# Kernel optimization log

Measured on AMD Instinct MI355X. Metric: run time of the kernel, lower is better.

The kernel has to match this reference:

```python
import jax, jax.numpy as jnp
import numpy as np

NV = 20000; NC = 20000; E = 500000
IN_SHAPE = 2; PE_DIM = 8; HID = 64; NL = 3
EPS = 1e-7  # GENConv message eps


def _lin(x, w, b):
    return x @ w + b


def _encode(x, pe, ew, eb, pw1, pb1, pw2, pb2):
    # relu(cat([Linear(x), 0.5*(pe_mlp(pe)+pe_mlp(-pe))], dim=1))
    def pe_mlp(p):
        return _lin(jax.nn.relu(_lin(p, pw1, pb1)), pw2, pb2)
    h = jnp.concatenate([_lin(x, ew, eb), 0.5 * (pe_mlp(pe) + pe_mlp(-pe))], axis=1)
    return jax.nn.relu(h)


def _genconv(x_src, x_dst, src, dst, ewt, lew, leb, w1, b1, w2, b2, n_dst):
    # GENConv(aggr='softmax', t=1, norm=None, msg_norm=False, edge_dim=1)
    msg = jax.nn.relu(x_src[src] + _lin(ewt, lew, leb)) + EPS  # [E, HID]
    m = jax.ops.segment_max(msg, dst, num_segments=n_dst)      # stable segment softmax
    ex = jnp.exp(msg - m[dst])
    s = jax.ops.segment_sum(ex, dst, num_segments=n_dst)
    agg = jax.ops.segment_sum(ex / (s[dst] + 1e-16) * msg, dst, num_segments=n_dst)
    out = agg + x_dst
    return _lin(jax.nn.relu(_lin(out, w1, b1)), w2, b2)  # MLP [hid -> 2hid -> hid]


def setup_inputs() -> dict:
    key = jax.random.key(0)
    ks = iter(jax.random.split(key, 64))
    d = {}
    d['x_vals'] = jax.random.normal(next(ks), (NV, IN_SHAPE), jnp.float32)
    d['x_cons'] = jax.random.normal(next(ks), (NC, IN_SHAPE), jnp.float32)
    d['pe_vals'] = jax.random.normal(next(ks), (NV, PE_DIM), jnp.float32)
    d['pe_cons'] = jax.random.normal(next(ks), (NC, PE_DIM), jnp.float32)
    d['edge_index_v2c'] = jnp.stack([
        jax.random.randint(next(ks), (E,), 0, NV),
        jax.random.randint(next(ks), (E,), 0, NC)])
    d['edge_index_c2v'] = jnp.stack([
        jax.random.randint(next(ks), (E,), 0, NC),
        jax.random.randint(next(ks), (E,), 0, NV)])
    d['edge_weight_v2c'] = jax.random.normal(next(ks), (E, 1), jnp.float32)
    d['edge_weight_c2v'] = jax.random.normal(next(ks), (E, 1), jnp.float32)
    def p(shape):
        return jax.random.normal(next(ks), shape, jnp.float32) * 0.05
    for k_ in ['vals', 'cons']:
        d[f'enc_{k_}_w'] = p((IN_SHAPE, HID // 2)); d[f'enc_{k_}_b'] = p((HID // 2,))
        d[f'pe_{k_}_w1'] = p((PE_DIM, HID)); d[f'pe_{k_}_b1'] = p((HID,))
        d[f'pe_{k_}_w2'] = p((HID, HID // 2)); d[f'pe_{k_}_b2'] = p((HID // 2,))
    for c in ['v2c', 'c2v']:
        d[f'{c}_edge_w'] = p((NL, 1, HID)); d[f'{c}_edge_b'] = p((NL, HID))
        d[f'{c}_w1'] = p((NL, HID, 2 * HID)); d[f'{c}_b1'] = p((NL, 2 * HID))
        d[f'{c}_w2'] = p((NL, 2 * HID, HID)); d[f'{c}_b2'] = p((NL, HID))
    for k_ in ['vals', 'cons']:
        d[f'pred_{k_}_w1'] = p((HID, HID)); d[f'pred_{k_}_b1'] = p((HID,))
        d[f'pred_{k_}_w2'] = p((HID, 1)); d[f'pred_{k_}_b2'] = p((1,))
    return d


def reference(x_vals, x_cons, pe_vals, pe_cons, edge_index_v2c, edge_index_c2v,
              edge_weight_v2c, edge_weight_c2v,
              enc_vals_w, enc_vals_b, pe_vals_w1, pe_vals_b1, pe_vals_w2, pe_vals_b2,
              enc_cons_w, enc_cons_b, pe_cons_w1, pe_cons_b1, pe_cons_w2, pe_cons_b2,
              v2c_edge_w, v2c_edge_b, v2c_w1, v2c_b1, v2c_w2, v2c_b2,
              c2v_edge_w, c2v_edge_b, c2v_w1, c2v_b1, c2v_w2, c2v_b2,
              pred_vals_w1, pred_vals_b1, pred_vals_w2, pred_vals_b2,
              pred_cons_w1, pred_cons_b1, pred_cons_w2, pred_cons_b2):
    vals = _encode(x_vals, pe_vals, enc_vals_w, enc_vals_b,
                   pe_vals_w1, pe_vals_b1, pe_vals_w2, pe_vals_b2)
    cons = _encode(x_cons, pe_cons, enc_cons_w, enc_cons_b,
                   pe_cons_w1, pe_cons_b1, pe_cons_w2, pe_cons_b2)
    hv, hc = [], []
    for i in range(NL):
        cons = _genconv(vals, cons, edge_index_v2c[0], edge_index_v2c[1],
                        edge_weight_v2c, v2c_edge_w[i], v2c_edge_b[i],
                        v2c_w1[i], v2c_b1[i], v2c_w2[i], v2c_b2[i], NC)
        vals = _genconv(cons, vals, edge_index_c2v[0], edge_index_c2v[1],
                        edge_weight_c2v, c2v_edge_w[i], c2v_edge_b[i],
                        c2v_w1[i], c2v_b1[i], c2v_w2[i], c2v_b2[i], NV)
        hc.append(cons); hv.append(vals)
    V = jnp.stack(hv)  # [NL, NV, HID]
    C = jnp.stack(hc)  # [NL, NC, HID]
    pv = _lin(jax.nn.relu(_lin(V, pred_vals_w1, pred_vals_b1)), pred_vals_w2, pred_vals_b2)
    pc = _lin(jax.nn.relu(_lin(C, pred_cons_w1, pred_cons_b1)), pred_cons_w2, pred_cons_b2)
    return pv[..., 0].T, pc[..., 0].T  # [NV, NL], [NC, NL]
```

## Files before the change

kernel.cpp:

```cpp
#include <hip/hip_runtime.h>

#define NVN 20000
#define NCN 20000
#define NE  500000
#define HID 64
#define NLAYER 3
#define TN 40
#define BSH 8
#define NB 79
#define P1E 2048

__device__ __forceinline__ float relu_(float x) { return fmaxf(x, 0.0f); }

__global__ __launch_bounds__(256) void binhist_kernel(
    const int* __restrict__ dstA, const int* __restrict__ dstB,
    int* __restrict__ binszA, int* __restrict__ binszB)
{
    __shared__ int cA[NB], cB[NB];
    int t = threadIdx.x;
    int e0 = blockIdx.x * P1E;
    if (t < NB) { cA[t] = 0; cB[t] = 0; }
    __syncthreads();
    for (int i = t; i < P1E; i += 256) {
        int e = e0 + i;
        if (e < NE) {
            atomicAdd(&cA[dstA[e] >> BSH], 1);
            atomicAdd(&cB[dstB[e] >> BSH], 1);
        }
    }
    __syncthreads();
    if (t < NB) {
        if (cA[t] > 0) atomicAdd(&binszA[t], cA[t]);
        if (cB[t] > 0) atomicAdd(&binszB[t], cB[t]);
    }
}

__global__ __launch_bounds__(256) void binscan_kernel(
    const int* __restrict__ binszA, int* __restrict__ binbaseA, int* __restrict__ bincurA,
    const int* __restrict__ binszB, int* __restrict__ binbaseB, int* __restrict__ bincurB)
{
    const int* binsz = blockIdx.x ? binszB : binszA;
    int* binbase     = blockIdx.x ? binbaseB : binbaseA;
    int* bincur      = blockIdx.x ? bincurB : bincurA;
    __shared__ int p[256];
    int t = threadIdx.x;
    p[t] = (t < NB) ? binsz[t] : 0;
    __syncthreads();
    for (int off = 1; off < 256; off <<= 1) {
        int v = (t >= off) ? p[t - off] : 0;
        __syncthreads();
        p[t] += v;
        __syncthreads();
    }
    if (t < NB) { int b = (t == 0) ? 0 : p[t - 1]; binbase[t] = b; bincur[t] = b; }
    if (t == NB) binbase[NB] = p[NB - 1];
}

__global__ __launch_bounds__(256) void scatter_p1_kernel(
    const int* __restrict__ eiA, const float* __restrict__ ewA,
    int* __restrict__ bincurA, int2* __restrict__ stageA,
    const int* __restrict__ eiB, const float* __restrict__ ewB,
    int* __restrict__ bincurB, int2* __restrict__ stageB)
{
    __shared__ int rnk[P1E];
    __shared__ int cnt[NB], base_[NB];
    int t = threadIdx.x;
    int e0 = blockIdx.x * P1E;

    for (int g = 0; g < 2; ++g) {
        const int* ei   = g ? eiB : eiA;
        const float* ew = g ? ewB : ewA;
        int* bincur     = g ? bincurB : bincurA;
        int2* stage     = g ? stageB : stageA;

        if (t < NB) cnt[t] = 0;
        __syncthreads();
        for (int i = t; i < P1E; i += 256) {
            int e = e0 + i;
            if (e < NE) {
                int d = ei[NE + e];
                rnk[i] = atomicAdd(&cnt[d >> BSH], 1);
            }
        }
        __syncthreads();
        if (t < NB && cnt[t] > 0) base_[t] = atomicAdd(&bincur[t], cnt[t]);
        __syncthreads();
        for (int i = t; i < P1E; i += 256) {
            int e = e0 + i;
            if (e < NE) {
                int s = ei[e], d = ei[NE + e];
                float w = ew[e];
                stage[base_[d >> BSH] + rnk[i]] =
                    make_int2((int)((unsigned)s | ((unsigned)d << 16)), __float_as_int(w));
            }
        }
        __syncthreads();
    }
}

__global__ __launch_bounds__(1024) void scatter_p2_kernel(
    const int* __restrict__ binbaseA, const int2* __restrict__ stageA,
    int* __restrict__ rowptrA, int2* __restrict__ pairA,
    const int* __restrict__ binbaseB, const int2* __restrict__ stageB,
    int* __restrict__ rowptrB, int2* __restrict__ pairB)
{
    __shared__ int deg[256], pfx[256], cur[256];
    int g = blockIdx.x / NB;
    int b = blockIdx.x % NB;
    const int* binbase = g ? binbaseB : binbaseA;
    const int2* stage  = g ? stageB : stageA;
    int* rowptr        = g ? rowptrB : rowptrA;
    int2* pair         = g ? pairB : pairA;

    int d0 = b << BSH;
    int d1 = min(d0 + 256, NCN);
    int nd = d1 - d0;
    int t = threadIdx.x;
    int estart = binbase[b], eend = binbase[b + 1];

    if (t < 256) deg[t] = 0;
    __syncthreads();
    for (int e = estart + t; e < eend; e += 1024) {
        int dst = (int)((unsigned)stage[e].x >> 16);
        atomicAdd(&deg[dst - d0], 1);
    }
    __syncthreads();
    if (t < 256) pfx[t] = deg[t];
    __syncthreads();
    for (int off = 1; off < 256; off <<= 1) {
        int v = (t >= off && t < 256) ? pfx[t - off] : 0;
        __syncthreads();
        if (t < 256) pfx[t] += v;
        __syncthreads();
    }
    if (t < nd) {
        int ex = estart + pfx[t] - deg[t];
        rowptr[d0 + t] = ex;
        cur[t] = ex;
    }
    if (t == 0) rowptr[d1] = eend;
    __syncthreads();
    for (int e = estart + t; e < eend; e += 1024) {
        int2 s = stage[e];
        unsigned u = (unsigned)s.x;
        int src = (int)(u & 0xFFFFu);
        int dst = (int)(u >> 16);
        int p = atomicAdd(&cur[dst - d0], 1);
        pair[p] = make_int2(src, s.y);
    }
}

__global__ __launch_bounds__(256) void encode2_kernel(
    const float* __restrict__ xv, const float* __restrict__ pev,
    const float* __restrict__ ewv, const float* __restrict__ ebv,
    const float* __restrict__ pw1v, const float* __restrict__ pb1v,
    const float* __restrict__ pw2v, const float* __restrict__ pb2v,
    const float* __restrict__ xc, const float* __restrict__ pec,
    const float* __restrict__ ewc, const float* __restrict__ ebc,
    const float* __restrict__ pw1c, const float* __restrict__ pb1c,
    const float* __restrict__ pw2c, const float* __restrict__ pb2c,
    float* __restrict__ outv, float* __restrict__ outc)
{
    __shared__ float sh[4][64];
    const int VB = (NVN + 3) / 4;
    int wave = threadIdx.x >> 6, lane = threadIdx.x & 63;
    int b = blockIdx.x;
    bool isC = (b >= VB);
    const float* x   = isC ? xc : xv;
    const float* pe  = isC ? pec : pev;
    const float* ew  = isC ? ewc : ewv;
    const float* eb  = isC ? ebc : ebv;
    const float* pw1 = isC ? pw1c : pw1v;
    const float* pb1 = isC ? pb1c : pb1v;
    const float* pw2 = isC ? pw2c : pw2v;
    const float* pb2 = isC ? pb2c : pb2v;
    float* out = isC ? outc : outv;
    int N = isC ? NCN : NVN;
    int n = (isC ? b - VB : b) * 4 + wave;
    if (n >= N) return;

    float accp = pb1[lane], accm = accp;
#pragma unroll
    for (int k = 0; k < 8; ++k) {
        float p = pe[n * 8 + k];
        float w = pw1[k * 64 + lane];
        accp += p * w;
        accm -= p * w;
    }
    float hs = 0.5f * (relu_(accp) + relu_(accm));
    float* my = sh[wave];
    my[lane] = hs;
    __builtin_amdgcn_wave_barrier();

    int col = lane & 31;
    float peo = pb2[col];
#pragma unroll
    for (int k = 0; k < 64; k += 4) {
        float4 hv = *(const float4*)(my + k);
        peo = fmaf(hv.x, pw2[(k + 0) * 32 + col], peo);
        peo = fmaf(hv.y, pw2[(k + 1) * 32 + col], peo);
        peo = fmaf(hv.z, pw2[(k + 2) * 32 + col], peo);
        peo = fmaf(hv.w, pw2[(k + 3) * 32 + col], peo);
    }
    float lino = x[n * 2 + 0] * ew[col] + x[n * 2 + 1] * ew[32 + col] + eb[col];
    float h = (lane < 32) ? lino : peo;
    out[n * 64 + lane] = relu_(h);
}

__global__ __launch_bounds__(256) void edge_agg_kernel(
    const float* __restrict__ xsrc,
    const float* __restrict__ xdst,
    const int* __restrict__ rowptr,
    const int2* __restrict__ pair,
    const float* __restrict__ lew,
    const float* __restrict__ leb,
    float* __restrict__ oa,
    int N)
{
    int wave = threadIdx.x >> 6, lane = threadIdx.x & 63;
    int n = blockIdx.x * 4 + wave;
    if (n >= N) return;

    int start = __builtin_amdgcn_readfirstlane(rowptr[n]);
    int end   = __builtin_amdgcn_readfirstlane(rowptr[n + 1]);
    float lw = lew[lane], lb = leb[lane];
    float xd = xdst[n * 64 + lane];

    float den = 0.0f, num = 0.0f;
    int j = start;

    if (j + 16 <= end) {
        int2 pb[16];
#pragma unroll
        for (int c = 0; c < 16; ++c) pb[c] = pair[j + c];

        for (; j + 32 <= end; j += 16) {
            float xv[16];
#pragma unroll
            for (int c = 0; c < 16; ++c) xv[c] = xsrc[pb[c].x * 64 + lane];
            int2 pn[16];
#pragma unroll
            for (int c = 0; c < 16; ++c) pn[c] = pair[j + 16 + c];
#pragma unroll
            for (int c = 0; c < 16; ++c) {
                float msg = relu_(fmaf(__int_as_float(pb[c].y), lw, xv[c] + lb)) + 1e-7f;
                float e = __expf(msg);
                den += e;
                num = fmaf(e, msg, num);
            }
#pragma unroll
            for (int c = 0; c < 16; ++c) pb[c] = pn[c];
        }
        {
            float xv[16];
#pragma unroll
            for (int c = 0; c < 16; ++c) xv[c] = xsrc[pb[c].x * 64 + lane];
#pragma unroll
            for (int c = 0; c < 16; ++c) {
                float msg = relu_(fmaf(__int_as_float(pb[c].y), lw, xv[c] + lb)) + 1e-7f;
                float e = __expf(msg);
                den += e;
                num = fmaf(e, msg, num);
            }
            j += 16;
        }
    }
    for (; j + 8 <= end; j += 8) {
        int2 p8[8];
#pragma unroll
        for (int c = 0; c < 8; ++c) p8[c] = pair[j + c];
        float xv[8];
#pragma unroll
        for (int c = 0; c < 8; ++c) xv[c] = xsrc[p8[c].x * 64 + lane];
#pragma unroll
        for (int c = 0; c < 8; ++c) {
            float msg = relu_(fmaf(__int_as_float(p8[c].y), lw, xv[c] + lb)) + 1e-7f;
            float e = __expf(msg);
            den += e;
            num = fmaf(e, msg, num);
        }
    }
    for (; j < end; ++j) {
        int2 p = pair[j];
        float xv = xsrc[p.x * 64 + lane];
        float msg = relu_(fmaf(__int_as_float(p.y), lw, xv + lb)) + 1e-7f;
        float e = __expf(msg);
        den += e;
        num = fmaf(e, msg, num);
    }

    oa[n * 64 + lane] = num / (den + 1e-16f) + xd;
}

__global__ __launch_bounds__(256) void mlp_kernel(
    const float* __restrict__ oa,
    float* __restrict__ feat,
    const float* __restrict__ w1,
    const float* __restrict__ b1,
    const float* __restrict__ w2,
    const float* __restrict__ b2,
    const float* __restrict__ pw1,
    const float* __restrict__ pb1,
    const float* __restrict__ pw2,
    const float* __restrict__ pb2,
    float* __restrict__ outp,
    int N, int layer)
{
    __shared__ float w1s[64 * 128];
    __shared__ float w2s[128 * 64];
    __shared__ float pw1s[64 * 64];
    __shared__ float b1s[128];
    __shared__ float b2s[64];
    __shared__ float pb1s[64];
    __shared__ float pw2s[64];
    __shared__ float act[TN][68];
    __shared__ float hid[TN][132];

    int tid = threadIdx.x;
    for (int i = tid; i < 64 * 128; i += 256) w1s[i] = w1[i];
    for (int i = tid; i < 128 * 64; i += 256) w2s[i] = w2[i];
    for (int i = tid; i < 64 * 64; i += 256) pw1s[i] = pw1[i];
    if (tid < 128) b1s[tid] = b1[tid];
    if (tid < 64) { b2s[tid] = b2[tid]; pb1s[tid] = pb1[tid]; pw2s[tid] = pw2[tid]; }
    float pb2v = pb2[0];

    int o4 = (tid & 31) * 4;
    int o2 = (tid & 31) * 2;
    int n5 = (tid >> 5) * 5;
    __syncthreads();

    int ntiles = N / TN;
    for (int tile = blockIdx.x; tile < ntiles; tile += gridDim.x) {
        int base = tile * TN;
        {
            const float* g = oa + (size_t)base * 64;
            for (int i = tid; i < TN * 64; i += 256)
                act[i >> 6][i & 63] = g[i];
        }
        __syncthreads();

        {
            float acc[5][4];
#pragma unroll
            for (int i = 0; i < 5; ++i)
#pragma unroll
                for (int q = 0; q < 4; ++q) acc[i][q] = b1s[o4 + q];
            for (int k = 0; k < 64; k += 4) {
                float4 a[5];
#pragma unroll
                for (int i = 0; i < 5; ++i) a[i] = *(const float4*)&act[n5 + i][k];
                float4 w0 = *(const float4*)&w1s[(k + 0) * 128 + o4];
                float4 wq1 = *(const float4*)&w1s[(k + 1) * 128 + o4];
                float4 wq2 = *(const float4*)&w1s[(k + 2) * 128 + o4];
                float4 wq3 = *(const float4*)&w1s[(k + 3) * 128 + o4];
#pragma unroll
                for (int i = 0; i < 5; ++i) {
                    acc[i][0] = fmaf(a[i].x, w0.x, acc[i][0]);
                    acc[i][1] = fmaf(a[i].x, w0.y, acc[i][1]);
                    acc[i][2] = fmaf(a[i].x, w0.z, acc[i][2]);
                    acc[i][3] = fmaf(a[i].x, w0.w, acc[i][3]);
                    acc[i][0] = fmaf(a[i].y, wq1.x, acc[i][0]);
                    acc[i][1] = fmaf(a[i].y, wq1.y, acc[i][1]);
                    acc[i][2] = fmaf(a[i].y, wq1.z, acc[i][2]);
                    acc[i][3] = fmaf(a[i].y, wq1.w, acc[i][3]);
                    acc[i][0] = fmaf(a[i].z, wq2.x, acc[i][0]);
                    acc[i][1] = fmaf(a[i].z, wq2.y, acc[i][1]);
                    acc[i][2] = fmaf(a[i].z, wq2.z, acc[i][2]);
                    acc[i][3] = fmaf(a[i].z, wq2.w, acc[i][3]);
                    acc[i][0] = fmaf(a[i].w, wq3.x, acc[i][0]);
                    acc[i][1] = fmaf(a[i].w, wq3.y, acc[i][1]);
                    acc[i][2] = fmaf(a[i].w, wq3.z, acc[i][2]);
                    acc[i][3] = fmaf(a[i].w, wq3.w, acc[i][3]);
                }
            }
#pragma unroll
            for (int i = 0; i < 5; ++i) {
                float4 h4 = make_float4(relu_(acc[i][0]), relu_(acc[i][1]),
                                        relu_(acc[i][2]), relu_(acc[i][3]));
                *(float4*)&hid[n5 + i][o4] = h4;
            }
        }
        __syncthreads();

        {
            float acc[5][2];
#pragma unroll
            for (int i = 0; i < 5; ++i) { acc[i][0] = b2s[o2]; acc[i][1] = b2s[o2 + 1]; }
            for (int k = 0; k < 128; k += 4) {
                float4 a[5];
#pragma unroll
                for (int i = 0; i < 5; ++i) a[i] = *(const float4*)&hid[n5 + i][k];
                float2 w0 = *(const float2*)&w2s[(k + 0) * 64 + o2];
                float2 wq1 = *(const float2*)&w2s[(k + 1) * 64 + o2];
                float2 wq2 = *(const float2*)&w2s[(k + 2) * 64 + o2];
                float2 wq3 = *(const float2*)&w2s[(k + 3) * 64 + o2];
#pragma unroll
                for (int i = 0; i < 5; ++i) {
                    acc[i][0] = fmaf(a[i].x, w0.x, acc[i][0]);
                    acc[i][1] = fmaf(a[i].x, w0.y, acc[i][1]);
                    acc[i][0] = fmaf(a[i].y, wq1.x, acc[i][0]);
                    acc[i][1] = fmaf(a[i].y, wq1.y, acc[i][1]);
                    acc[i][0] = fmaf(a[i].z, wq2.x, acc[i][0]);
                    acc[i][1] = fmaf(a[i].z, wq2.y, acc[i][1]);
                    acc[i][0] = fmaf(a[i].w, wq3.x, acc[i][0]);
                    acc[i][1] = fmaf(a[i].w, wq3.y, acc[i][1]);
                }
            }
#pragma unroll
            for (int i = 0; i < 5; ++i) {
                float2 r2 = make_float2(acc[i][0], acc[i][1]);
                *(float2*)&feat[(size_t)(base + n5 + i) * 64 + o2] = r2;
                *(float2*)&act[n5 + i][o2] = r2;
            }
        }
        __syncthreads();

        {
            float acc[5][2];
#pragma unroll
            for (int i = 0; i < 5; ++i) { acc[i][0] = pb1s[o2]; acc[i][1] = pb1s[o2 + 1]; }
            for (int k = 0; k < 64; k += 4) {
                float4 a[5];
#pragma unroll
                for (int i = 0; i < 5; ++i) a[i] = *(const float4*)&act[n5 + i][k];
                float2 w0 = *(const float2*)&pw1s[(k + 0) * 64 + o2];
                float2 wq1 = *(const float2*)&pw1s[(k + 1) * 64 + o2];
                float2 wq2 = *(const float2*)&pw1s[(k + 2) * 64 + o2];
                float2 wq3 = *(const float2*)&pw1s[(k + 3) * 64 + o2];
#pragma unroll
                for (int i = 0; i < 5; ++i) {
                    acc[i][0] = fmaf(a[i].x, w0.x, acc[i][0]);
                    acc[i][1] = fmaf(a[i].x, w0.y, acc[i][1]);
                    acc[i][0] = fmaf(a[i].y, wq1.x, acc[i][0]);
                    acc[i][1] = fmaf(a[i].y, wq1.y, acc[i][1]);
                    acc[i][0] = fmaf(a[i].z, wq2.x, acc[i][0]);
                    acc[i][1] = fmaf(a[i].z, wq2.y, acc[i][1]);
                    acc[i][0] = fmaf(a[i].w, wq3.x, acc[i][0]);
                    acc[i][1] = fmaf(a[i].w, wq3.y, acc[i][1]);
                }
            }
            float pw2a = pw2s[o2], pw2b = pw2s[o2 + 1];
            float ps[5];
#pragma unroll
            for (int i = 0; i < 5; ++i)
                ps[i] = relu_(acc[i][0]) * pw2a + relu_(acc[i][1]) * pw2b;
#pragma unroll
            for (int msk = 16; msk >= 1; msk >>= 1) {
#pragma unroll
                for (int i = 0; i < 5; ++i)
                    ps[i] += __shfl_xor(ps[i], msk, 64);
            }
            if ((tid & 31) == 0) {
#pragma unroll
                for (int i = 0; i < 5; ++i)
                    outp[(size_t)(base + n5 + i) * NLAYER + layer] = ps[i] + pb2v;
            }
        }
        __syncthreads();
    }
}

extern "C" void kernel_launch(void* const* d_in, const int* in_sizes, int n_in,
                              void* d_out, int out_size, void* d_ws, size_t ws_size,
                              hipStream_t stream)
{
    const float* x_vals   = (const float*)d_in[0];
    const float* x_cons   = (const float*)d_in[1];
    const float* pe_vals  = (const float*)d_in[2];
    const float* pe_cons  = (const float*)d_in[3];
    const int*   ei_v2c   = (const int*)d_in[4];
    const int*   ei_c2v   = (const int*)d_in[5];
    const float* ew_v2c   = (const float*)d_in[6];
    const float* ew_c2v   = (const float*)d_in[7];
    const float* enc_vals_w = (const float*)d_in[8];
    const float* enc_vals_b = (const float*)d_in[9];
    const float* pe_vals_w1 = (const float*)d_in[10];
    const float* pe_vals_b1 = (const float*)d_in[11];
    const float* pe_vals_w2 = (const float*)d_in[12];
    const float* pe_vals_b2 = (const float*)d_in[13];
    const float* enc_cons_w = (const float*)d_in[14];
    const float* enc_cons_b = (const float*)d_in[15];
    const float* pe_cons_w1 = (const float*)d_in[16];
    const float* pe_cons_b1 = (const float*)d_in[17];
    const float* pe_cons_w2 = (const float*)d_in[18];
    const float* pe_cons_b2 = (const float*)d_in[19];
    const float* v2c_edge_w = (const float*)d_in[20];
    const float* v2c_edge_b = (const float*)d_in[21];
    const float* v2c_w1     = (const float*)d_in[22];
    const float* v2c_b1     = (const float*)d_in[23];
    const float* v2c_w2     = (const float*)d_in[24];
    const float* v2c_b2     = (const float*)d_in[25];
    const float* c2v_edge_w = (const float*)d_in[26];
    const float* c2v_edge_b = (const float*)d_in[27];
    const float* c2v_w1     = (const float*)d_in[28];
    const float* c2v_b1     = (const float*)d_in[29];
    const float* c2v_w2     = (const float*)d_in[30];
    const float* c2v_b2     = (const float*)d_in[31];
    const float* pred_vals_w1 = (const float*)d_in[32];
    const float* pred_vals_b1 = (const float*)d_in[33];
    const float* pred_vals_w2 = (const float*)d_in[34];
    const float* pred_vals_b2 = (const float*)d_in[35];
    const float* pred_cons_w1 = (const float*)d_in[36];
    const float* pred_cons_b1 = (const float*)d_in[37];
    const float* pred_cons_w2 = (const float*)d_in[38];
    const float* pred_cons_b2 = (const float*)d_in[39];

    float* out = (float*)d_out;
    float* out_c = out + (size_t)NVN * NLAYER;

    const size_t NF = (size_t)NVN * 64;

    float* ws     = (float*)d_ws;
    float* feat_v = ws;
    float* feat_c = feat_v + NF;
    float* oa     = feat_c + NF;
    int2* v2c_pair  = (int2*)(oa + NF);
    int2* c2v_pair  = v2c_pair + NE;
    int2* v2c_stage = c2v_pair + NE;
    int2* c2v_stage = v2c_stage + NE;
    int* ip = (int*)(c2v_stage + NE);
    int* v2c_binsz   = ip; ip += NB;
    int* c2v_binsz   = ip; ip += NB;
    int* v2c_binbase = ip; ip += NB + 1;
    int* c2v_binbase = ip; ip += NB + 1;
    int* v2c_bincur  = ip; ip += NB;
    int* c2v_bincur  = ip; ip += NB;
    int* v2c_rowptr  = ip; ip += NCN + 1;
    int* c2v_rowptr  = ip; ip += NVN + 1;

    const int p1b = (NE + P1E - 1) / P1E;

    hipMemsetAsync(v2c_binsz, 0, (size_t)(2 * NB) * sizeof(int), stream);
    binhist_kernel<<<p1b, 256, 0, stream>>>(ei_v2c + NE, ei_c2v + NE,
                                            v2c_binsz, c2v_binsz);
    binscan_kernel<<<2, 256, 0, stream>>>(v2c_binsz, v2c_binbase, v2c_bincur,
                                          c2v_binsz, c2v_binbase, c2v_bincur);
    scatter_p1_kernel<<<p1b, 256, 0, stream>>>(
        ei_v2c, ew_v2c, v2c_bincur, v2c_stage,
        ei_c2v, ew_c2v, c2v_bincur, c2v_stage);
    scatter_p2_kernel<<<2 * NB, 1024, 0, stream>>>(
        v2c_binbase, v2c_stage, v2c_rowptr, v2c_pair,
        c2v_binbase, c2v_stage, c2v_rowptr, c2v_pair);

    encode2_kernel<<<(NVN + 3) / 4 + (NCN + 3) / 4, 256, 0, stream>>>(
        x_vals, pe_vals, enc_vals_w, enc_vals_b,
        pe_vals_w1, pe_vals_b1, pe_vals_w2, pe_vals_b2,
        x_cons, pe_cons, enc_cons_w, enc_cons_b,
        pe_cons_w1, pe_cons_b1, pe_cons_w2, pe_cons_b2,
        feat_v, feat_c);

    for (int i = 0; i < NLAYER; ++i) {
        edge_agg_kernel<<<(NCN + 3) / 4, 256, 0, stream>>>(
            feat_v, feat_c, v2c_rowptr, v2c_pair,
            v2c_edge_w + (size_t)i * HID, v2c_edge_b + (size_t)i * HID,
            oa, NCN);
        mlp_kernel<<<250, 256, 0, stream>>>(
            oa, feat_c,
            v2c_w1 + (size_t)i * 8192, v2c_b1 + (size_t)i * 128,
            v2c_w2 + (size_t)i * 8192, v2c_b2 + (size_t)i * 64,
            pred_cons_w1, pred_cons_b1, pred_cons_w2, pred_cons_b2,
            out_c, NCN, i);
        edge_agg_kernel<<<(NVN + 3) / 4, 256, 0, stream>>>(
            feat_c, feat_v, c2v_rowptr, c2v_pair,
            c2v_edge_w + (size_t)i * HID, c2v_edge_b + (size_t)i * HID,
            oa, NVN);
        mlp_kernel<<<250, 256, 0, stream>>>(
            oa, feat_v,
            c2v_w1 + (size_t)i * 8192, c2v_b1 + (size_t)i * 128,
            c2v_w2 + (size_t)i * 8192, c2v_b2 + (size_t)i * 64,
            pred_vals_w1, pred_vals_b1, pred_vals_w2, pred_vals_b2,
            out, NVN, i);
    }
}
```

Before: 485.5 us.

## Read MLP weights from global/L1 instead of LDS and double MLP grid

The MLP kernel stops staging the three weight matrices (about 80KB) in shared memory and reads them directly from global memory, relying on the cache. This cuts LDS use to roughly 35KB so more blocks fit per CU, and removes the per-block weight preload that each of the 250 blocks paid. The grid goes from 250 to 500 blocks (one 40-node tile each), launch bounds request 4 blocks per CU, activation loads are vectorised to float4, and the k loops get unroll 2. The risk is that the weight reads in the inner loops now go through the vector memory path instead of LDS, which may add latency.

```diff
diff --git a/kernel.cpp b/kernel.cpp
--- a/kernel.cpp
+++ b/kernel.cpp
@@ -292,7 +292,7 @@
     oa[n * 64 + lane] = num / (den + 1e-16f) + xd;
 }
 
-__global__ __launch_bounds__(256) void mlp_kernel(
+__global__ __launch_bounds__(256, 4) void mlp_kernel(
     const float* __restrict__ oa,
     float* __restrict__ feat,
     const float* __restrict__ w1,
@@ -306,20 +306,14 @@
     float* __restrict__ outp,
     int N, int layer)
 {
-    __shared__ float w1s[64 * 128];
-    __shared__ float w2s[128 * 64];
-    __shared__ float pw1s[64 * 64];
+    __shared__ float act[TN][68];
+    __shared__ float hid[TN][132];
     __shared__ float b1s[128];
     __shared__ float b2s[64];
     __shared__ float pb1s[64];
     __shared__ float pw2s[64];
-    __shared__ float act[TN][68];
-    __shared__ float hid[TN][132];
 
     int tid = threadIdx.x;
-    for (int i = tid; i < 64 * 128; i += 256) w1s[i] = w1[i];
-    for (int i = tid; i < 128 * 64; i += 256) w2s[i] = w2[i];
-    for (int i = tid; i < 64 * 64; i += 256) pw1s[i] = pw1[i];
     if (tid < 128) b1s[tid] = b1[tid];
     if (tid < 64) { b2s[tid] = b2[tid]; pb1s[tid] = pb1[tid]; pw2s[tid] = pw2[tid]; }
     float pb2v = pb2[0];
@@ -333,9 +327,9 @@
     for (int tile = blockIdx.x; tile < ntiles; tile += gridDim.x) {
         int base = tile * TN;
         {
-            const float* g = oa + (size_t)base * 64;
-            for (int i = tid; i < TN * 64; i += 256)
-                act[i >> 6][i & 63] = g[i];
+            const float4* g4 = (const float4*)(oa + (size_t)base * 64);
+            for (int i = tid; i < TN * 16; i += 256)
+                *(float4*)&act[i >> 4][(i & 15) * 4] = g4[i];
         }
         __syncthreads();
 
@@ -345,14 +339,15 @@
             for (int i = 0; i < 5; ++i)
 #pragma unroll
                 for (int q = 0; q < 4; ++q) acc[i][q] = b1s[o4 + q];
+#pragma unroll 2
             for (int k = 0; k < 64; k += 4) {
                 float4 a[5];
 #pragma unroll
                 for (int i = 0; i < 5; ++i) a[i] = *(const float4*)&act[n5 + i][k];
-                float4 w0 = *(const float4*)&w1s[(k + 0) * 128 + o4];
-                float4 wq1 = *(const float4*)&w1s[(k + 1) * 128 + o4];
-                float4 wq2 = *(const float4*)&w1s[(k + 2) * 128 + o4];
-                float4 wq3 = *(const float4*)&w1s[(k + 3) * 128 + o4];
+                float4 w0 = *(const float4*)&w1[(k + 0) * 128 + o4];
+                float4 wq1 = *(const float4*)&w1[(k + 1) * 128 + o4];
+                float4 wq2 = *(const float4*)&w1[(k + 2) * 128 + o4];
+                float4 wq3 = *(const float4*)&w1[(k + 3) * 128 + o4];
 #pragma unroll
                 for (int i = 0; i < 5; ++i) {
                     acc[i][0] = fmaf(a[i].x, w0.x, acc[i][0]);
@@ -386,14 +381,15 @@
             float acc[5][2];
 #pragma unroll
             for (int i = 0; i < 5; ++i) { acc[i][0] = b2s[o2]; acc[i][1] = b2s[o2 + 1]; }
+#pragma unroll 2
             for (int k = 0; k < 128; k += 4) {
                 float4 a[5];
 #pragma unroll
                 for (int i = 0; i < 5; ++i) a[i] = *(const float4*)&hid[n5 + i][k];
-                float2 w0 = *(const float2*)&w2s[(k + 0) * 64 + o2];
-                float2 wq1 = *(const float2*)&w2s[(k + 1) * 64 + o2];
-                float2 wq2 = *(const float2*)&w2s[(k + 2) * 64 + o2];
-                float2 wq3 = *(const float2*)&w2s[(k + 3) * 64 + o2];
+                float2 w0 = *(const float2*)&w2[(k + 0) * 64 + o2];
+                float2 wq1 = *(const float2*)&w2[(k + 1) * 64 + o2];
+                float2 wq2 = *(const float2*)&w2[(k + 2) * 64 + o2];
+                float2 wq3 = *(const float2*)&w2[(k + 3) * 64 + o2];
 #pragma unroll
                 for (int i = 0; i < 5; ++i) {
                     acc[i][0] = fmaf(a[i].x, w0.x, acc[i][0]);
@@ -419,14 +415,15 @@
             float acc[5][2];
 #pragma unroll
             for (int i = 0; i < 5; ++i) { acc[i][0] = pb1s[o2]; acc[i][1] = pb1s[o2 + 1]; }
+#pragma unroll 2
             for (int k = 0; k < 64; k += 4) {
                 float4 a[5];
 #pragma unroll
                 for (int i = 0; i < 5; ++i) a[i] = *(const float4*)&act[n5 + i][k];
-                float2 w0 = *(const float2*)&pw1s[(k + 0) * 64 + o2];
-                float2 wq1 = *(const float2*)&pw1s[(k + 1) * 64 + o2];
-                float2 wq2 = *(const float2*)&pw1s[(k + 2) * 64 + o2];
-                float2 wq3 = *(const float2*)&pw1s[(k + 3) * 64 + o2];
+                float2 w0 = *(const float2*)&pw1[(k + 0) * 64 + o2];
+                float2 wq1 = *(const float2*)&pw1[(k + 1) * 64 + o2];
+                float2 wq2 = *(const float2*)&pw1[(k + 2) * 64 + o2];
+                float2 wq3 = *(const float2*)&pw1[(k + 3) * 64 + o2];
 #pragma unroll
                 for (int i = 0; i < 5; ++i) {
                     acc[i][0] = fmaf(a[i].x, w0.x, acc[i][0]);
@@ -554,7 +551,7 @@
             feat_v, feat_c, v2c_rowptr, v2c_pair,
             v2c_edge_w + (size_t)i * HID, v2c_edge_b + (size_t)i * HID,
             oa, NCN);
-        mlp_kernel<<<250, 256, 0, stream>>>(
+        mlp_kernel<<<500, 256, 0, stream>>>(
             oa, feat_c,
             v2c_w1 + (size_t)i * 8192, v2c_b1 + (size_t)i * 128,
             v2c_w2 + (size_t)i * 8192, v2c_b2 + (size_t)i * 64,
@@ -564,7 +561,7 @@
             feat_c, feat_v, c2v_rowptr, c2v_pair,
             c2v_edge_w + (size_t)i * HID, c2v_edge_b + (size_t)i * HID,
             oa, NVN);
-        mlp_kernel<<<250, 256, 0, stream>>>(
+        mlp_kernel<<<500, 256, 0, stream>>>(
             oa, feat_v,
             c2v_w1 + (size_t)i * 8192, c2v_b1 + (size_t)i * 128,
             c2v_w2 + (size_t)i * 8192, c2v_b2 + (size_t)i * 64,
```

After: 435.3 us. -10.3%, faster.
